# Performance work log

Hardware: AMD Instinct MI355X
Metric: run time of the kernel (lower is better)

The kernel has to match this reference:

```python
import jax, jax.numpy as jnp
import numpy as np

DIM = 2048; KV_RANK = 512; Q_RANK = 768; H = 16
D_NR = 128; D_R = 64; D_V = 128
B = 8; L = 32; MAX_T = 4096; START = MAX_T - L
QK_DIM = D_NR + D_R
SCALE = 1.0 / float(np.sqrt(QK_DIM))
EPS = 1.1920929e-07  # torch.finfo(float32).eps (nn.RMSNorm default)
ROPE_BASE = 10000.0


def rms_norm(x, w):
    return x * jax.lax.rsqrt(jnp.mean(x * x, axis=-1, keepdims=True) + EPS) * w


def apply_rope(x, cos, sin):
    # x: (b, l, h, d) with d even; cos/sin: (l, d//2) -> complex multiply on pairs
    b, l, h, d = x.shape
    xp = x.reshape(b, l, h, d // 2, 2)
    xr, xi = xp[..., 0], xp[..., 1]
    c = cos[None, :, None, :]
    s = sin[None, :, None, :]
    return jnp.stack([xr * c - xi * s, xr * s + xi * c], axis=-1).reshape(b, l, h, d)


def setup_inputs() -> dict:
    key = jax.random.key(0)
    ks = jax.random.split(key, 9)
    w = 0.02
    # rotary angles for absolute positions START..START+L-1
    inv_freq = 1.0 / (ROPE_BASE ** (np.arange(0, D_R, 2, dtype=np.float32) / D_R))  # (32,)
    pos = np.arange(START, START + L, dtype=np.float32)
    ang = pos[:, None] * inv_freq[None, :]  # (L, 32)
    # causal mask over full cache: query i sits at absolute position START+i
    t = jnp.arange(MAX_T)[None, :]
    qpos = START + jnp.arange(L)[:, None]
    mask = jnp.where(t <= qpos, 0.0, -1e30).astype(jnp.float32)  # (L, MAX_T)
    return {
        "x": jax.random.normal(ks[0], (B, L, DIM), dtype=jnp.float32),
        "start_pos": START,
        "freq_cos": jnp.asarray(np.cos(ang), dtype=jnp.float32),
        "freq_sin": jnp.asarray(np.sin(ang), dtype=jnp.float32),
        "mask": mask,
        "kv_latent_cache": jax.random.normal(ks[1], (B, MAX_T, KV_RANK), dtype=jnp.float32) * 0.05,
        "k_rope_cache": jax.random.normal(ks[2], (B, MAX_T, D_R), dtype=jnp.float32) * 0.05,
        "w_kv_down": jax.random.normal(ks[3], (KV_RANK + D_R, DIM), dtype=jnp.float32) * w,
        "w_q_down": jax.random.normal(ks[4], (Q_RANK, DIM), dtype=jnp.float32) * w,
        "rms_q_w": jnp.ones((Q_RANK,), dtype=jnp.float32),
        "w_q_up": jax.random.normal(ks[5], (H * QK_DIM, Q_RANK), dtype=jnp.float32) * w,
        "w_kv_up": jax.random.normal(ks[6], (H * (D_NR + D_V), KV_RANK), dtype=jnp.float32) * w,
        "w_out": jax.random.normal(ks[7], (DIM, H * D_V), dtype=jnp.float32) * w,
    }


def reference(x, start_pos, freq_cos, freq_sin, mask, kv_latent_cache, k_rope_cache,
              w_kv_down, w_q_down, rms_q_w, w_q_up, w_kv_up, w_out):
    b, l, _ = x.shape
    end_pos = start_pos + l
    # query path: down-proj -> RMSNorm -> up-proj (NOTE: module's rms_norm_kv is unused)
    q = rms_norm(x @ w_q_down.T, rms_q_w) @ w_q_up.T
    q = q.reshape(b, l, H, QK_DIM)
    q_nrope, q_rope = q[..., :D_NR], q[..., D_NR:]
    q_rope = apply_rope(q_rope, freq_cos, freq_sin)
    # latent kv path
    kv = x @ w_kv_down.T  # (b, l, KV_RANK + D_R)
    kv_latent, k_rope = kv[..., :KV_RANK], kv[..., KV_RANK:]
    k_rope = apply_rope(k_rope[:, :, None, :], freq_cos, freq_sin)[:, :, 0, :]
    # scatter-write into caches, then read prefix [:end_pos]
    kvc = kv_latent_cache.at[:, start_pos:end_pos].set(kv_latent)[:, :end_pos]  # (b, t, k)
    krc = k_rope_cache.at[:, start_pos:end_pos].set(k_rope)[:, :end_pos]        # (b, t, r)
    # weight absorption
    w_up = w_kv_up.reshape(H, D_NR + D_V, KV_RANK)
    q_abs = jnp.einsum('blhd,hdk->blhk', q_nrope, w_up[:, :D_NR])
    scores = (jnp.einsum('blhk,btk->blht', q_abs, kvc)
              + jnp.einsum('blhr,btr->blht', q_rope, krc)) * SCALE
    scores = scores + mask[None, :, None, :]
    p = jax.nn.softmax(scores, axis=-1)
    o = jnp.einsum('blht,btk->blhk', p, kvc)
    o = jnp.einsum('blhk,hdk->blhd', o, w_up[:, D_NR:])
    return o.reshape(b, l, H * D_V) @ w_out.T
```

## Files before the change

kernel.cpp:

```cpp
#include <hip/hip_runtime.h>
#include <math.h>

#define DIMX 2048
#define KV_RANK 512
#define Q_RANK 768
#define NH 16
#define D_NR 128
#define D_R 64
#define D_V 128
#define NB 8
#define NL 32
#define MAX_T 4096
#define STARTP (MAX_T - NL)
#define QK_DIM (D_NR + D_R)
#define ATT_SCALE 0.07216878364870323f
#define RMS_EPS 1.1920929e-07f

typedef unsigned short u16;
typedef __attribute__((ext_vector_type(4))) unsigned short u16x4;
typedef __attribute__((ext_vector_type(8))) short short8;
typedef __attribute__((ext_vector_type(4))) float f32x4;

#define GLOBAL_AS __attribute__((address_space(1)))
#define LDS_AS __attribute__((address_space(3)))

#define NDOWN 1344
#define DPART ((long long)256 * NDOWN)

__device__ inline u16 f2b(float f) {
    union { float f; unsigned u; } v; v.f = f;
    unsigned r = (v.u + 0x7fffu + ((v.u >> 16) & 1u)) >> 16;
    return (u16)r;
}
__device__ inline float b2f(u16 u) {
    union { unsigned u; float f; } v; v.u = ((unsigned)u) << 16; return v.f;
}

template<int BM, int BN, bool OUTB, bool GSWZ>
__global__ __launch_bounds__(256) void gemm_mfma(
    const u16* __restrict__ A, const u16* __restrict__ B, void* __restrict__ Cv,
    int K, int lda, int ldb, int ldc,
    long long sA1, long long sA2, long long sB1, long long sB2,
    long long sC1, long long sC2, int nb2)
{
    constexpr int MFR = BM / 32;
    constexpr int NFR = BN / 32;
    int bx = blockIdx.x, by = blockIdx.y, bz = blockIdx.z;
    if (GSWZ) {
        int flat = bx + gridDim.x * (by + gridDim.y * bz);
        int nwg = gridDim.x * gridDim.y * gridDim.z;
        int lf = (flat & 7) * (nwg >> 3) + (flat >> 3);
        bx = lf % gridDim.x;
        int r = lf / gridDim.x;
        by = r % gridDim.y;
        bz = r / gridDim.y;
    }
    const int z1 = bz / nb2, z2 = bz % nb2;
    A += z1 * sA1 + z2 * sA2;
    B += z1 * sB1 + z2 * sB2;

    const int m0 = by * BM;
    const int n0 = bx * BN;
    const int tid = threadIdx.x;
    const int lane = tid & 63;
    const int wid = tid >> 6;
    const int wm = wid >> 1, wn = wid & 1;
    const int l15 = lane & 15;
    const int l4  = lane >> 4;

    __shared__ __align__(16) u16 As[BM * 32];
    __shared__ __align__(16) u16 Bs[BN * 32];

    f32x4 acc[MFR][NFR];
    #pragma unroll
    for (int i = 0; i < MFR; ++i)
        #pragma unroll
        for (int j = 0; j < NFR; ++j)
            acc[i][j] = (f32x4)0.0f;

    constexpr int nA = BM / 16;
    constexpr int nB = BN / 16;

    for (int k0 = 0; k0 < K; k0 += 32) {
        #pragma unroll
        for (int j = 0; j < nA / 4 + 1; ++j) {
            int jj = wid + j * 4;
            if (jj < nA) {
                int c = jj * 64 + lane;
                const u16* src = A + (long long)(m0 + (c >> 2)) * lda + k0 + (c & 3) * 8;
                u16* dst = &As[jj * 512];
                __builtin_amdgcn_global_load_lds((const GLOBAL_AS void*)src,
                                                 (LDS_AS void*)dst, 16, 0, 0);
            }
        }
        #pragma unroll
        for (int j = 0; j < nB / 4 + 1; ++j) {
            int jj = wid + j * 4;
            if (jj < nB) {
                int c = jj * 64 + lane;
                const u16* src = B + (long long)(n0 + (c >> 2)) * ldb + k0 + (c & 3) * 8;
                u16* dst = &Bs[jj * 512];
                __builtin_amdgcn_global_load_lds((const GLOBAL_AS void*)src,
                                                 (LDS_AS void*)dst, 16, 0, 0);
            }
        }
        __syncthreads();

        short8 a[MFR], b[NFR];
        #pragma unroll
        for (int mf = 0; mf < MFR; ++mf)
            a[mf] = *(const short8*)&As[(wm * 16 * MFR + mf * 16 + l15) * 32 + l4 * 8];
        #pragma unroll
        for (int nf = 0; nf < NFR; ++nf)
            b[nf] = *(const short8*)&Bs[(wn * 16 * NFR + nf * 16 + l15) * 32 + l4 * 8];
        #pragma unroll
        for (int mf = 0; mf < MFR; ++mf)
            #pragma unroll
            for (int nf = 0; nf < NFR; ++nf)
                acc[mf][nf] = __builtin_amdgcn_mfma_f32_16x16x32_bf16(
                    a[mf], b[nf], acc[mf][nf], 0, 0, 0);
        __syncthreads();
    }

    if (OUTB) {
        u16* C = (u16*)Cv + z1 * sC1 + z2 * sC2;
        #pragma unroll
        for (int mf = 0; mf < MFR; ++mf)
            #pragma unroll
            for (int nf = 0; nf < NFR; ++nf) {
                int r0 = m0 + wm * 16 * MFR + mf * 16 + l4 * 4;
                int c0 = n0 + wn * 16 * NFR + nf * 16 + l15;
                #pragma unroll
                for (int r = 0; r < 4; ++r)
                    C[(long long)(r0 + r) * ldc + c0] = f2b(acc[mf][nf][r]);
            }
    } else {
        float* C = (float*)Cv + z1 * sC1 + z2 * sC2;
        #pragma unroll
        for (int mf = 0; mf < MFR; ++mf)
            #pragma unroll
            for (int nf = 0; nf < NFR; ++nf) {
                int r0 = m0 + wm * 16 * MFR + mf * 16 + l4 * 4;
                int c0 = n0 + wn * 16 * NFR + nf * 16 + l15;
                #pragma unroll
                for (int r = 0; r < 4; ++r)
                    C[(long long)(r0 + r) * ldc + c0] = acc[mf][nf][r];
            }
    }
}

struct Segs {
    const float* src[6];
    u16* dst[6];
    int n4[6];
};
__global__ __launch_bounds__(256) void f2b_multi(Segs s)
{
    int seg = blockIdx.y;
    int i = blockIdx.x * 256 + threadIdx.x;
    if (i >= s.n4[seg]) return;
    float4 v = ((const float4*)s.src[seg])[i];
    u16x4 o = { f2b(v.x), f2b(v.y), f2b(v.z), f2b(v.w) };
    ((u16x4*)s.dst[seg])[i] = o;
}

__global__ __launch_bounds__(256) void rms_reduce(const float* __restrict__ part,
                                                  const float* __restrict__ w,
                                                  u16* __restrict__ outb)
{
    const int row = blockIdx.x;
    const int tid = threadIdx.x;
    __shared__ float red[256];
    float val[3];
    float s = 0.f;
    #pragma unroll
    for (int j = 0; j < 3; ++j) {
        int i = tid + j * 256;
        long long off = (long long)row * NDOWN + i;
        float v = part[off] + part[DPART + off] + part[2 * DPART + off] + part[3 * DPART + off];
        val[j] = v;
        s += v * v;
    }
    red[tid] = s; __syncthreads();
    for (int off = 128; off > 0; off >>= 1) {
        if (tid < off) red[tid] += red[tid + off];
        __syncthreads();
    }
    float scale = rsqrtf(red[0] / (float)Q_RANK + RMS_EPS);
    u16* ob = outb + (long long)row * Q_RANK;
    #pragma unroll
    for (int j = 0; j < 3; ++j) {
        int i = tid + j * 256;
        ob[i] = f2b(val[j] * scale * w[i]);
    }
}

__global__ __launch_bounds__(256) void wuT_kernel(const float* __restrict__ w,
                                                  u16* __restrict__ outp)
{
    __shared__ u16 T[64][65];
    const int h = blockIdx.z;
    const int y0 = blockIdx.y * 64;
    const int x0 = blockIdx.x * 64;
    const int tid = threadIdx.x;
    #pragma unroll
    for (int i = 0; i < 16; ++i) {
        int lin = i * 256 + tid;
        int r = lin >> 6, c = lin & 63;
        T[c][r] = f2b(w[((long long)h * 256 + y0 + r) * 512 + x0 + c]);
    }
    __syncthreads();
    #pragma unroll
    for (int i = 0; i < 16; ++i) {
        int lin = i * 256 + tid;
        int r = lin >> 6, c = lin & 63;
        outp[((long long)h * 512 + x0 + r) * 128 + y0 + c] = T[r][c];
    }
}

__global__ __launch_bounds__(256) void bcat_new_reduce(const float* __restrict__ part,
                                                       const float* __restrict__ fc,
                                                       const float* __restrict__ fs,
                                                       u16* __restrict__ bcat)
{
    const int bl = blockIdx.x;
    const int b = bl >> 5, l = bl & 31;
    const int t = threadIdx.x;
    if (t >= 144) return;
    long long off = (long long)bl * NDOWN + 768 + 4 * t;
    float4 v0 = *(const float4*)(part + off);
    float4 v1 = *(const float4*)(part + DPART + off);
    float4 v2 = *(const float4*)(part + 2 * DPART + off);
    float4 v3 = *(const float4*)(part + 3 * DPART + off);
    float4 v = { v0.x + v1.x + v2.x + v3.x, v0.y + v1.y + v2.y + v3.y,
                 v0.z + v1.z + v2.z + v3.z, v0.w + v1.w + v2.w + v3.w };
    u16* dst = bcat + ((long long)b * MAX_T + STARTP + l) * 576;
    if (t < 128) {
        u16x4 o = { f2b(v.x), f2b(v.y), f2b(v.z), f2b(v.w) };
        ((u16x4*)dst)[t] = o;
    } else {
        int g = t - 128;
        float c0 = fc[l * 32 + 2 * g],     s0 = fs[l * 32 + 2 * g];
        float c1 = fc[l * 32 + 2 * g + 1], s1 = fs[l * 32 + 2 * g + 1];
        u16x4 o = { f2b(v.x * c0 - v.y * s0), f2b(v.x * s0 + v.y * c0),
                    f2b(v.z * c1 - v.w * s1), f2b(v.z * s1 + v.w * c1) };
        *(u16x4*)(dst + 512 + 4 * g) = o;
    }
}

__global__ __launch_bounds__(256) void prep_cache(const float* __restrict__ kvc,
                                                  const float* __restrict__ krc,
                                                  u16* __restrict__ bcat,
                                                  u16* __restrict__ kvcT)
{
    const int b = blockIdx.z;
    const int t0 = blockIdx.y * 64;
    const int tid = threadIdx.x;

    if (blockIdx.x == 8) {
        #pragma unroll
        for (int i = 0; i < 4; ++i) {
            int lin = i * 256 + tid;
            int r = lin >> 4, c4 = lin & 15;
            int t = t0 + r;
            if (t >= STARTP) continue;
            float4 v = ((const float4*)(krc + ((long long)b * MAX_T + t) * D_R))[c4];
            u16x4 o = { f2b(v.x), f2b(v.y), f2b(v.z), f2b(v.w) };
            *(u16x4*)(bcat + ((long long)b * MAX_T + t) * 576 + 512 + 4 * c4) = o;
        }
        return;
    }

    __shared__ u16 T[64 * 64];
    const int k0 = blockIdx.x * 64;

    #pragma unroll
    for (int i = 0; i < 4; ++i) {
        int lin = i * 256 + tid;
        int r = lin >> 4, c4 = lin & 15;
        int t = t0 + r;
        u16x4 o;
        if (t < STARTP) {
            float4 v = *(const float4*)(kvc + ((long long)b * MAX_T + t) * KV_RANK + k0 + 4 * c4);
            o.x = f2b(v.x); o.y = f2b(v.y); o.z = f2b(v.z); o.w = f2b(v.w);
            *(u16x4*)(bcat + ((long long)b * MAX_T + t) * 576 + k0 + 4 * c4) = o;
        } else {
            o = *(const u16x4*)(bcat + ((long long)b * MAX_T + t) * 576 + k0 + 4 * c4);
        }
        int tg = r >> 2, te = r & 3;
        int col = ((tg ^ c4) << 2) + te;
        #pragma unroll
        for (int j = 0; j < 4; ++j)
            T[(4 * c4 + j) * 64 + col] = o[j];
    }
    __syncthreads();

    u16* outp = kvcT + ((long long)b * KV_RANK + k0) * MAX_T + t0;
    #pragma unroll
    for (int i = 0; i < 4; ++i) {
        int lin = i * 256 + tid;
        int k = lin >> 4, c4 = lin & 15;
        u16x4 v = *(const u16x4*)&T[k * 64 + ((c4 ^ (k >> 2)) << 2)];
        *(u16x4*)(outp + (long long)k * MAX_T + 4 * c4) = v;
    }
}

__global__ __launch_bounds__(256) void rope_q(const u16* __restrict__ qb,
                                              const float* __restrict__ fc,
                                              const float* __restrict__ fs,
                                              u16* __restrict__ qprimeb)
{
    int idx = blockIdx.x * 256 + threadIdx.x;
    int i = idx & 31;
    int h = (idx >> 5) & (NH - 1);
    int l = (idx >> 9) & (NL - 1);
    int b = idx >> 14;
    const u16* src = qb + (long long)(b * NL + l) * 3072 + h * QK_DIM + D_NR + 2 * i;
    float xr = b2f(src[0]), xi = b2f(src[1]);
    float c = fc[l * 32 + i], s = fs[l * 32 + i];
    u16* dst = qprimeb + ((long long)(b * NH + h) * NL + l) * 576 + 512 + 2 * i;
    dst[0] = f2b(xr * c - xi * s);
    dst[1] = f2b(xr * s + xi * c);
}

__global__ __launch_bounds__(256) void softmax_bf16(float* __restrict__ scores)
{
    const int row = blockIdx.x;
    const int l = row & 31;
    const int vlen = STARTP + l + 1;
    float* s = scores + (long long)row * MAX_T;
    __shared__ float red[256];
    const int tid = threadIdx.x;

    float4 v[4];
    float m = -1e30f;
    #pragma unroll
    for (int i = 0; i < 4; ++i) {
        int f4 = i * 256 + tid;
        v[i] = ((const float4*)s)[f4];
        int t = f4 * 4;
        if (t + 0 >= vlen) v[i].x = -1e30f;
        if (t + 1 >= vlen) v[i].y = -1e30f;
        if (t + 2 >= vlen) v[i].z = -1e30f;
        if (t + 3 >= vlen) v[i].w = -1e30f;
        m = fmaxf(m, fmaxf(fmaxf(v[i].x, v[i].y), fmaxf(v[i].z, v[i].w)));
    }
    red[tid] = m; __syncthreads();
    for (int off = 128; off > 0; off >>= 1) {
        if (tid < off) red[tid] = fmaxf(red[tid], red[tid + off]);
        __syncthreads();
    }
    const float mm = red[0] * ATT_SCALE;
    __syncthreads();

    float sum = 0.f;
    #pragma unroll
    for (int i = 0; i < 4; ++i) {
        v[i].x = __expf(v[i].x * ATT_SCALE - mm);
        v[i].y = __expf(v[i].y * ATT_SCALE - mm);
        v[i].z = __expf(v[i].z * ATT_SCALE - mm);
        v[i].w = __expf(v[i].w * ATT_SCALE - mm);
        sum += v[i].x + v[i].y + v[i].z + v[i].w;
    }
    red[tid] = sum; __syncthreads();
    for (int off = 128; off > 0; off >>= 1) {
        if (tid < off) red[tid] += red[tid + off];
        __syncthreads();
    }
    const float inv = 1.0f / red[0];
    u16* ps = (u16*)s;
    #pragma unroll
    for (int i = 0; i < 4; ++i) {
        int f4 = i * 256 + tid;
        u16x4 o = { f2b(v[i].x * inv), f2b(v[i].y * inv), f2b(v[i].z * inv), f2b(v[i].w * inv) };
        ((u16x4*)ps)[f4] = o;
    }
}

__global__ __launch_bounds__(256) void reduce_pv(const float* __restrict__ part,
                                                 u16* __restrict__ o_hb)
{
    int idx = blockIdx.x * 256 + threadIdx.x;
    int b = idx >> 16;
    int i4 = idx & 65535;
    const float* p = part + (long long)b * 1048576 + 4 * i4;
    float4 v0 = *(const float4*)p;
    float4 v1 = *(const float4*)(p + 262144);
    float4 v2 = *(const float4*)(p + 524288);
    float4 v3 = *(const float4*)(p + 786432);
    u16x4 o = { f2b(v0.x + v1.x + v2.x + v3.x), f2b(v0.y + v1.y + v2.y + v3.y),
                f2b(v0.z + v1.z + v2.z + v3.z), f2b(v0.w + v1.w + v2.w + v3.w) };
    ((u16x4*)(o_hb + (long long)b * 262144))[i4] = o;
}

__global__ __launch_bounds__(256) void reduce_out(const float* __restrict__ part,
                                                  float* __restrict__ out)
{
    int idx = blockIdx.x * 256 + threadIdx.x;
    const float* p = part + 4 * (long long)idx;
    float4 v0 = *(const float4*)p;
    float4 v1 = *(const float4*)(p + 524288);
    float4 v2 = *(const float4*)(p + 1048576);
    float4 v3 = *(const float4*)(p + 1572864);
    float4 o = { v0.x + v1.x + v2.x + v3.x, v0.y + v1.y + v2.y + v3.y,
                 v0.z + v1.z + v2.z + v3.z, v0.w + v1.w + v2.w + v3.w };
    ((float4*)out)[idx] = o;
}

extern "C" void kernel_launch(void* const* d_in, const int* in_sizes, int n_in,
                              void* d_out, int out_size, void* d_ws, size_t ws_size,
                              hipStream_t stream)
{
    const float* x        = (const float*)d_in[0];
    const float* fc       = (const float*)d_in[2];
    const float* fs       = (const float*)d_in[3];
    const float* kvc      = (const float*)d_in[5];
    const float* krc      = (const float*)d_in[6];
    const float* w_kv_down= (const float*)d_in[7];
    const float* w_q_down = (const float*)d_in[8];
    const float* rms_q_w  = (const float*)d_in[9];
    const float* w_q_up   = (const float*)d_in[10];
    const float* w_kv_up  = (const float*)d_in[11];
    const float* w_out    = (const float*)d_in[12];
    float* out            = (float*)d_out;

    float* down_part = (float*)d_ws;
    float* scores  = down_part + 1376256;
    u16* base      = (u16*)(scores + 16777216);
    u16* xb      = base;                 base += 524288;
    u16* qdb     = base;                 base += 196608;
    u16* qb      = base;                 base += 786432;
    u16* qprimeb = base;                 base += 2359296;
    u16* wqkv_b  = base;                 base += 2752512;
    u16* wqu_b   = base;                 base += 2359296;
    u16* wkvu_b  = base;                 base += 2097152;
    u16* wout_b  = base;                 base += 4194304;
    u16* wuT     = base;                 base += 1048576;
    u16* bcat    = base;                 base += 18874368;
    u16* kvcT    = base;                 base += 16777216;
    u16* o_hb    = base;                 base += 2097152;
    u16* o_upb   = base;                 base += 524288;
    float* pv_part  = (float*)bcat;
    float* out_part = (float*)kvcT;

    Segs segs;
    segs.src[0] = x;         segs.dst[0] = xb;                  segs.n4[0] = 131072;
    segs.src[1] = w_q_down;  segs.dst[1] = wqkv_b;              segs.n4[1] = 393216;
    segs.src[2] = w_q_up;    segs.dst[2] = wqu_b;               segs.n4[2] = 589824;
    segs.src[3] = w_kv_down; segs.dst[3] = wqkv_b + 768 * 2048; segs.n4[3] = 294912;
    segs.src[4] = w_kv_up;   segs.dst[4] = wkvu_b;              segs.n4[4] = 524288;
    segs.src[5] = w_out;     segs.dst[5] = wout_b;              segs.n4[5] = 1048576;
    f2b_multi<<<dim3(4096, 6), 256, 0, stream>>>(segs);

    wuT_kernel<<<dim3(8, 2, 16), 256, 0, stream>>>(w_kv_up, wuT);

    gemm_mfma<32, 64, false, true><<<dim3(21, 8, 4), 256, 0, stream>>>(
        xb, wqkv_b, down_part, 512, 2048, 2048, NDOWN,
        0LL, 512LL, 0LL, 512LL, 0LL, DPART, 4);
    rms_reduce<<<256, 256, 0, stream>>>(down_part, rms_q_w, qdb);
    gemm_mfma<32, 64, true, true><<<dim3(48, 8, 1), 256, 0, stream>>>(
        qdb, wqu_b, qb, 768, 768, 768, 3072, 0, 0, 0, 0, 0, 0, 1);
    bcat_new_reduce<<<256, 256, 0, stream>>>(down_part, fc, fs, bcat);
    prep_cache<<<dim3(9, 64, 8), 256, 0, stream>>>(kvc, krc, bcat, kvcT);

    gemm_mfma<32, 128, true, true><<<dim3(4, 1, 128), 256, 0, stream>>>(
        qb, wuT, qprimeb, 128, 3072, 128, 576,
        98304LL, 192LL, 0LL, 65536LL, 294912LL, 18432LL, 16);
    rope_q<<<512, 256, 0, stream>>>(qb, fc, fs, qprimeb);

    gemm_mfma<128, 128, false, true><<<dim3(32, 4, 8), 256, 0, stream>>>(
        qprimeb, bcat, scores, 576, 576, 576, 4096,
        294912LL, 0LL, 2359296LL, 0LL, 2097152LL, 0LL, 1);
    softmax_bf16<<<NB * NH * NL, 256, 0, stream>>>(scores);
    gemm_mfma<128, 128, false, true><<<dim3(4, 4, 32), 256, 0, stream>>>(
        (const u16*)scores, kvcT, pv_part, 1024, 8192, 4096, 512,
        4194304LL, 1024LL, 2097152LL, 1024LL, 1048576LL, 262144LL, 4);
    reduce_pv<<<2048, 256, 0, stream>>>(pv_part, o_hb);

    gemm_mfma<32, 64, true, true><<<dim3(2, 1, 128), 256, 0, stream>>>(
        o_hb, wkvu_b + 128 * 512, o_upb, 512, 512, 512, 2048,
        262144LL, 16384LL, 0LL, 131072LL, 65536LL, 128LL, 16);
    gemm_mfma<32, 64, false, true><<<dim3(32, 8, 4), 256, 0, stream>>>(
        o_upb, wout_b, out_part, 512, 2048, 2048, 2048,
        0LL, 512LL, 0LL, 512LL, 0LL, 524288LL, 4);
    reduce_out<<<512, 256, 0, stream>>>(out_part, out);
}
```

Baseline: 323.1 us.

## Fuse softmax exponentiation into QK score GEMM epilogue, defer normalization

The score GEMM now writes exp(scaled score) directly as bf16 with causal masking and accumulates per-row sums through atomics into a small buffer. The standalone softmax kernel is removed, and the division by the row sum moves into the PV partial-sum reduction. This drops the fp32 score matrix round trip and one kernel launch. There is no max subtraction, so the result relies on scores staying small enough not to overflow exp, and the atomics make the row sums nondeterministic in order.

New measurement: 325.9 us. No clear change (+0.9%).

```diff
diff --git a/kernel.cpp b/kernel.cpp
--- a/kernel.cpp
+++ b/kernel.cpp
@@ -36,9 +36,10 @@
     union { unsigned u; float f; } v; v.u = ((unsigned)u) << 16; return v.f;
 }
 
-template<int BM, int BN, bool OUTB, bool GSWZ>
+template<int BM, int BN, int OUTMODE, bool GSWZ>
 __global__ __launch_bounds__(256) void gemm_mfma(
     const u16* __restrict__ A, const u16* __restrict__ B, void* __restrict__ Cv,
+    float* __restrict__ rs,
     int K, int lda, int ldb, int ldc,
     long long sA1, long long sA2, long long sB1, long long sB2,
     long long sC1, long long sC2, int nb2)
@@ -122,7 +123,46 @@
         __syncthreads();
     }
 
-    if (OUTB) {
+    if (OUTMODE == 2) {
+        u16* C = (u16*)Cv + z1 * sC1 + z2 * sC2;
+        float rowp[MFR][4];
+        #pragma unroll
+        for (int mf = 0; mf < MFR; ++mf)
+            #pragma unroll
+            for (int r = 0; r < 4; ++r)
+                rowp[mf][r] = 0.f;
+        #pragma unroll
+        for (int mf = 0; mf < MFR; ++mf) {
+            #pragma unroll
+            for (int nf = 0; nf < NFR; ++nf) {
+                int r0 = m0 + wm * 16 * MFR + mf * 16 + l4 * 4;
+                int c0 = n0 + wn * 16 * NFR + nf * 16 + l15;
+                #pragma unroll
+                for (int r = 0; r < 4; ++r) {
+                    int row = r0 + r;
+                    int vlen = STARTP + (row & 31) + 1;
+                    float p = (c0 < vlen) ? __expf(acc[mf][nf][r] * ATT_SCALE) : 0.f;
+                    u16 pb = f2b(p);
+                    C[(long long)row * ldc + c0] = pb;
+                    rowp[mf][r] += b2f(pb);
+                }
+            }
+        }
+        #pragma unroll
+        for (int mf = 0; mf < MFR; ++mf)
+            #pragma unroll
+            for (int r = 0; r < 4; ++r) {
+                float v = rowp[mf][r];
+                v += __shfl_xor(v, 1);
+                v += __shfl_xor(v, 2);
+                v += __shfl_xor(v, 4);
+                v += __shfl_xor(v, 8);
+                if (l15 == 0) {
+                    int row = m0 + wm * 16 * MFR + mf * 16 + l4 * 4 + r;
+                    atomicAdd(&rs[z1 * 512 + row], v);
+                }
+            }
+    } else if (OUTMODE == 1) {
         u16* C = (u16*)Cv + z1 * sC1 + z2 * sC2;
         #pragma unroll
         for (int mf = 0; mf < MFR; ++mf)
@@ -162,6 +202,13 @@
     float4 v = ((const float4*)s.src[seg])[i];
     u16x4 o = { f2b(v.x), f2b(v.y), f2b(v.z), f2b(v.w) };
     ((u16x4*)s.dst[seg])[i] = o;
+}
+
+__global__ __launch_bounds__(256) void rs_zero(float* __restrict__ rs)
+{
+    int i = blockIdx.x * 256 + threadIdx.x;
+    float4 z = { 0.f, 0.f, 0.f, 0.f };
+    ((float4*)rs)[i] = z;
 }
 
 __global__ __launch_bounds__(256) void rms_reduce(const float* __restrict__ part,
@@ -323,73 +370,24 @@
     dst[1] = f2b(xr * s + xi * c);
 }
 
-__global__ __launch_bounds__(256) void softmax_bf16(float* __restrict__ scores)
-{
-    const int row = blockIdx.x;
-    const int l = row & 31;
-    const int vlen = STARTP + l + 1;
-    float* s = scores + (long long)row * MAX_T;
-    __shared__ float red[256];
-    const int tid = threadIdx.x;
-
-    float4 v[4];
-    float m = -1e30f;
-    #pragma unroll
-    for (int i = 0; i < 4; ++i) {
-        int f4 = i * 256 + tid;
-        v[i] = ((const float4*)s)[f4];
-        int t = f4 * 4;
-        if (t + 0 >= vlen) v[i].x = -1e30f;
-        if (t + 1 >= vlen) v[i].y = -1e30f;
-        if (t + 2 >= vlen) v[i].z = -1e30f;
-        if (t + 3 >= vlen) v[i].w = -1e30f;
-        m = fmaxf(m, fmaxf(fmaxf(v[i].x, v[i].y), fmaxf(v[i].z, v[i].w)));
-    }
-    red[tid] = m; __syncthreads();
-    for (int off = 128; off > 0; off >>= 1) {
-        if (tid < off) red[tid] = fmaxf(red[tid], red[tid + off]);
-        __syncthreads();
-    }
-    const float mm = red[0] * ATT_SCALE;
-    __syncthreads();
-
-    float sum = 0.f;
-    #pragma unroll
-    for (int i = 0; i < 4; ++i) {
-        v[i].x = __expf(v[i].x * ATT_SCALE - mm);
-        v[i].y = __expf(v[i].y * ATT_SCALE - mm);
-        v[i].z = __expf(v[i].z * ATT_SCALE - mm);
-        v[i].w = __expf(v[i].w * ATT_SCALE - mm);
-        sum += v[i].x + v[i].y + v[i].z + v[i].w;
-    }
-    red[tid] = sum; __syncthreads();
-    for (int off = 128; off > 0; off >>= 1) {
-        if (tid < off) red[tid] += red[tid + off];
-        __syncthreads();
-    }
-    const float inv = 1.0f / red[0];
-    u16* ps = (u16*)s;
-    #pragma unroll
-    for (int i = 0; i < 4; ++i) {
-        int f4 = i * 256 + tid;
-        u16x4 o = { f2b(v[i].x * inv), f2b(v[i].y * inv), f2b(v[i].z * inv), f2b(v[i].w * inv) };
-        ((u16x4*)ps)[f4] = o;
-    }
-}
-
 __global__ __launch_bounds__(256) void reduce_pv(const float* __restrict__ part,
+                                                 const float* __restrict__ rs,
                                                  u16* __restrict__ o_hb)
 {
     int idx = blockIdx.x * 256 + threadIdx.x;
     int b = idx >> 16;
     int i4 = idx & 65535;
+    int m = i4 >> 7;
     const float* p = part + (long long)b * 1048576 + 4 * i4;
     float4 v0 = *(const float4*)p;
     float4 v1 = *(const float4*)(p + 262144);
     float4 v2 = *(const float4*)(p + 524288);
     float4 v3 = *(const float4*)(p + 786432);
-    u16x4 o = { f2b(v0.x + v1.x + v2.x + v3.x), f2b(v0.y + v1.y + v2.y + v3.y),
-                f2b(v0.z + v1.z + v2.z + v3.z), f2b(v0.w + v1.w + v2.w + v3.w) };
+    float inv = 1.0f / rs[b * 512 + m];
+    u16x4 o = { f2b((v0.x + v1.x + v2.x + v3.x) * inv),
+                f2b((v0.y + v1.y + v2.y + v3.y) * inv),
+                f2b((v0.z + v1.z + v2.z + v3.z) * inv),
+                f2b((v0.w + v1.w + v2.w + v3.w) * inv) };
     ((u16x4*)(o_hb + (long long)b * 262144))[i4] = o;
 }
 
@@ -425,8 +423,9 @@
     float* out            = (float*)d_out;
 
     float* down_part = (float*)d_ws;
-    float* scores  = down_part + 1376256;
-    u16* base      = (u16*)(scores + 16777216);
+    float* rs      = down_part + 1376256;
+    u16* pb        = (u16*)(rs + 4096);
+    u16* base      = pb + 16777216;
     u16* xb      = base;                 base += 524288;
     u16* qdb     = base;                 base += 196608;
     u16* qb      = base;                 base += 786432;
@@ -452,36 +451,36 @@
     segs.src[5] = w_out;     segs.dst[5] = wout_b;              segs.n4[5] = 1048576;
     f2b_multi<<<dim3(4096, 6), 256, 0, stream>>>(segs);
 
+    rs_zero<<<4, 256, 0, stream>>>(rs);
     wuT_kernel<<<dim3(8, 2, 16), 256, 0, stream>>>(w_kv_up, wuT);
 
-    gemm_mfma<32, 64, false, true><<<dim3(21, 8, 4), 256, 0, stream>>>(
-        xb, wqkv_b, down_part, 512, 2048, 2048, NDOWN,
+    gemm_mfma<32, 64, 0, true><<<dim3(21, 8, 4), 256, 0, stream>>>(
+        xb, wqkv_b, down_part, nullptr, 512, 2048, 2048, NDOWN,
         0LL, 512LL, 0LL, 512LL, 0LL, DPART, 4);
     rms_reduce<<<256, 256, 0, stream>>>(down_part, rms_q_w, qdb);
-    gemm_mfma<32, 64, true, true><<<dim3(48, 8, 1), 256, 0, stream>>>(
-        qdb, wqu_b, qb, 768, 768, 768, 3072, 0, 0, 0, 0, 0, 0, 1);
+    gemm_mfma<32, 64, 1, true><<<dim3(48, 8, 1), 256, 0, stream>>>(
+        qdb, wqu_b, qb, nullptr, 768, 768, 768, 3072, 0, 0, 0, 0, 0, 0, 1);
     bcat_new_reduce<<<256, 256, 0, stream>>>(down_part, fc, fs, bcat);
     prep_cache<<<dim3(9, 64, 8), 256, 0, stream>>>(kvc, krc, bcat, kvcT);
 
-    gemm_mfma<32, 128, true, true><<<dim3(4, 1, 128), 256, 0, stream>>>(
-        qb, wuT, qprimeb, 128, 3072, 128, 576,
+    gemm_mfma<32, 128, 1, true><<<dim3(4, 1, 128), 256, 0, stream>>>(
+        qb, wuT, qprimeb, nullptr, 128, 3072, 128, 576,
         98304LL, 192LL, 0LL, 65536LL, 294912LL, 18432LL, 16);
     rope_q<<<512, 256, 0, stream>>>(qb, fc, fs, qprimeb);
 
-    gemm_mfma<128, 128, false, true><<<dim3(32, 4, 8), 256, 0, stream>>>(
-        qprimeb, bcat, scores, 576, 576, 576, 4096,
+    gemm_mfma<128, 128, 2, true><<<dim3(32, 4, 8), 256, 0, stream>>>(
+        qprimeb, bcat, pb, rs, 576, 576, 576, 4096,
         294912LL, 0LL, 2359296LL, 0LL, 2097152LL, 0LL, 1);
-    softmax_bf16<<<NB * NH * NL, 256, 0, stream>>>(scores);
-    gemm_mfma<128, 128, false, true><<<dim3(4, 4, 32), 256, 0, stream>>>(
-        (const u16*)scores, kvcT, pv_part, 1024, 8192, 4096, 512,
-        4194304LL, 1024LL, 2097152LL, 1024LL, 1048576LL, 262144LL, 4);
-    reduce_pv<<<2048, 256, 0, stream>>>(pv_part, o_hb);
-
-    gemm_mfma<32, 64, true, true><<<dim3(2, 1, 128), 256, 0, stream>>>(
-        o_hb, wkvu_b + 128 * 512, o_upb, 512, 512, 512, 2048,
+    gemm_mfma<128, 128, 0, true><<<dim3(4, 4, 32), 256, 0, stream>>>(
+        pb, kvcT, pv_part, nullptr, 1024, 4096, 4096, 512,
+        2097152LL, 1024LL, 2097152LL, 1024LL, 1048576LL, 262144LL, 4);
+    reduce_pv<<<2048, 256, 0, stream>>>(pv_part, rs, o_hb);
+
+    gemm_mfma<32, 64, 1, true><<<dim3(2, 1, 128), 256, 0, stream>>>(
+        o_hb, wkvu_b + 128 * 512, o_upb, nullptr, 512, 512, 512, 2048,
         262144LL, 16384LL, 0LL, 131072LL, 65536LL, 128LL, 16);
-    gemm_mfma<32, 64, false, true><<<dim3(32, 8, 4), 256, 0, stream>>>(
-        o_upb, wout_b, out_part, 512, 2048, 2048, 2048,
+    gemm_mfma<32, 64, 0, true><<<dim3(32, 8, 4), 256, 0, stream>>>(
+        o_upb, wout_b, out_part, nullptr, 512, 2048, 2048, 2048,
         0LL, 512LL, 0LL, 512LL, 0LL, 524288LL, 4);
     reduce_out<<<512, 256, 0, stream>>>(out_part, out);
 }
```
